# Performance work log

Hardware: AMD Instinct MI355X
Metric: run time of the kernel (lower is better)

Reference implementation:

```python
import jax, jax.numpy as jnp
import numpy as np

B, L, IN_DIM, DIM, H = 1, 256, 128, 32, 4
LN_EPS = 1e-5


def setup_inputs() -> dict:
    key = jax.random.key(0)
    ks = jax.random.split(key, 7)
    z = jax.random.normal(ks[0], (B, L, L, IN_DIM), dtype=jnp.float32)
    src_mask = jax.random.randint(ks[1], (B, L), 0, 2, dtype=jnp.int32)
    ln_g = jnp.ones((IN_DIM,), jnp.float32)
    ln_b = jnp.zeros((IN_DIM,), jnp.float32)
    w_qkv = jax.random.normal(ks[2], (IN_DIM, 3 * H * DIM), jnp.float32) * 0.02
    w_pair = jax.random.normal(ks[3], (IN_DIM, H), jnp.float32) * 0.02
    w_gate = jax.random.normal(ks[4], (IN_DIM, IN_DIM), jnp.float32) * 0.02
    b_gate = jnp.zeros((IN_DIM,), jnp.float32)
    w_out = jax.random.normal(ks[5], (H * DIM, IN_DIM), jnp.float32) * 0.02
    b_out = jnp.zeros((IN_DIM,), jnp.float32)
    return dict(z=z, src_mask=src_mask, ln_g=ln_g, ln_b=ln_b, w_qkv=w_qkv,
                w_pair=w_pair, w_gate=w_gate, b_gate=b_gate, w_out=w_out, b_out=b_out)


def reference(z, src_mask, ln_g, ln_b, w_qkv, w_pair, w_gate, b_gate, w_out, b_out):
    # mask: 0 -> -1, then outer product -> (B, L, L) with entries in {-1, +1}
    m = jnp.where(src_mask == 0, -1, src_mask).astype(jnp.float32)
    attn_mask = m[:, :, None] * m[:, None, :]                      # (B, L, L)

    # LayerNorm over feature dim (biased variance, as torch)
    mu = jnp.mean(z, axis=-1, keepdims=True)
    var = jnp.mean((z - mu) ** 2, axis=-1, keepdims=True)
    zn = (z - mu) / jnp.sqrt(var + LN_EPS) * ln_g + ln_b           # (B, I, J, C)

    gate = jax.nn.sigmoid(zn @ w_gate + b_gate)                    # (B, I, J, C)
    bias = zn @ w_pair                                             # (B, I, J, H)

    qkv = zn @ w_qkv                                               # (B, I, J, 3*H*D)
    q, k, v = jnp.split(qkv, 3, axis=-1)
    q = q.reshape(B, L, L, H, DIM)
    k = k.reshape(B, L, L, H, DIM)
    v = v.reshape(B, L, L, H, DIM)

    # NOTE: original code DIVIDES by scale = d**-0.5 (i.e. multiplies by sqrt(d)).
    scale = DIM ** (-0.5)
    logits = jnp.einsum('brihd,brjhd->brijh', q, k) / scale        # (B, R, I, J, H)
    logits = logits + bias[:, None, :, :, :]
    # NOTE: original masked_fill uses -1e-9 (tiny), kept faithfully.
    logits = jnp.where(attn_mask[:, None, :, :, None] == -1, jnp.float32(-1e-9), logits)
    attn = jax.nn.softmax(logits, axis=3)                          # softmax over key j

    out = jnp.einsum('brijh,brjhd->brihd', attn, v)                # (B, R, I, H, D)
    out = out.reshape(B, L, L, H * DIM)
    return (gate * out) @ w_out + b_out                            # (B, I, J, C)
```

## Files before the change

### kernel.cpp

```cpp
#include <hip/hip_runtime.h>
#include <hip/hip_bf16.h>

#define L_DIM 256
#define C_DIM 128
#define H_DIM 4
#define NPOS (L_DIM * L_DIM)
#define SQRT_D 5.6568542494923806f

typedef float f32x4 __attribute__((ext_vector_type(4)));
typedef short bf16x8 __attribute__((ext_vector_type(8)));
typedef unsigned short ushort8_t __attribute__((ext_vector_type(8)));

__device__ __forceinline__ float bf2f(unsigned short u) {
  return __uint_as_float(((unsigned)u) << 16);
}
__device__ __forceinline__ unsigned short f2bf(float f) {
  unsigned u = __float_as_uint(f);
  unsigned r = u + 0x7fffu + ((u >> 16) & 1u);
  return (unsigned short)(r >> 16);
}

__global__ __launch_bounds__(256)
void k_prep(const float* __restrict__ w_qkv, const float* __restrict__ w_gate,
            const float* __restrict__ w_out,
            unsigned short* __restrict__ WcS, unsigned short* __restrict__ WoT) {
  int idx = blockIdx.x * 256 + threadIdx.x;
  if (idx < 4 * 128 * 128) {
    int h = idx >> 14, rem = idx & 16383, rr = rem >> 7, c = rem & 127;
    int o = rr >> 5, n32 = rr & 31;
    float v = (o < 3) ? w_qkv[c * 384 + o * 128 + h * 32 + n32]
                      : w_gate[c * 128 + h * 32 + n32];
    int byte_in_row = (2 * c) ^ ((rr & 7) << 4);
    WcS[h * 16384 + rr * 128 + (byte_in_row >> 1)] = f2bf(v);
  } else if (idx < 4 * 128 * 128 + 128 * 128) {
    int i2 = idx - 65536;
    int n = i2 >> 7, c = i2 & 127;
    WoT[i2] = f2bf(w_out[c * 128 + n]);
  }
}

__global__ __launch_bounds__(256)
void k_bias(const float* __restrict__ z, const float* __restrict__ ln_g,
            const float* __restrict__ ln_b, const float* __restrict__ w_pair,
            float* __restrict__ biasT) {
  int t = threadIdx.x;
  int p = blockIdx.x * 32 + (t >> 3);
  int lane = t & 7;
  const float* zp = &z[(size_t)p * C_DIM + lane * 16];
  float x[16];
  #pragma unroll
  for (int e = 0; e < 4; e++) {
    float4 v = reinterpret_cast<const float4*>(zp)[e];
    x[e * 4 + 0] = v.x; x[e * 4 + 1] = v.y; x[e * 4 + 2] = v.z; x[e * 4 + 3] = v.w;
  }
  float s = 0.f;
  #pragma unroll
  for (int e = 0; e < 16; e++) s += x[e];
  s += __shfl_xor(s, 1); s += __shfl_xor(s, 2); s += __shfl_xor(s, 4);
  float mu = s * (1.0f / C_DIM);
  float v2 = 0.f;
  #pragma unroll
  for (int e = 0; e < 16; e++) { float d = x[e] - mu; v2 += d * d; }
  v2 += __shfl_xor(v2, 1); v2 += __shfl_xor(v2, 2); v2 += __shfl_xor(v2, 4);
  float rs = rsqrtf(v2 * (1.0f / C_DIM) + 1e-5f);
  float bh[H_DIM] = {};
  #pragma unroll
  for (int e = 0; e < 16; e++) {
    int c = lane * 16 + e;
    float zn = (x[e] - mu) * rs * ln_g[c] + ln_b[c];
    #pragma unroll
    for (int h = 0; h < H_DIM; h++) bh[h] += zn * w_pair[c * H_DIM + h];
  }
  #pragma unroll
  for (int h = 0; h < H_DIM; h++) {
    bh[h] += __shfl_xor(bh[h], 1); bh[h] += __shfl_xor(bh[h], 2); bh[h] += __shfl_xor(bh[h], 4);
  }
  if (lane == 0) {
    int iz = p >> 8, jz = p & 255;
    #pragma unroll
    for (int h = 0; h < H_DIM; h++) biasT[h * NPOS + jz * L_DIM + iz] = bh[h];
  }
}

__global__ __launch_bounds__(1024)
void k_fused(const float* __restrict__ z, const int* __restrict__ src_mask,
             const float* __restrict__ ln_g, const float* __restrict__ ln_b,
             const float* __restrict__ b_gate, const unsigned short* __restrict__ WcS,
             const float* __restrict__ biasT, float* __restrict__ og) {
  __shared__ __align__(16) char smem[156672];
  char* zn_c = smem;
  unsigned short* Qs = (unsigned short*)(smem);
  unsigned short* Ks = (unsigned short*)(smem + 20480);
  char* Vt_c = smem + 40960;
  char* P_c0 = smem + 57344;
  char* Wt_c = smem + 90112;
  int*  smk  = (int*)(smem + 155648);

  const int t = threadIdx.x;
  const int wave = t >> 6, lane = t & 63;
  const int l15 = lane & 15, l4 = lane >> 4;
  const int rbase = blockIdx.x * L_DIM;
  const int wrow0 = wave * 16;
  char* P_c = P_c0 + wave * 2048;

  {
    int ln8 = t & 7;
    #pragma unroll
    for (int pass = 0; pass < 2; ++pass) {
      int pos = pass * 128 + (t >> 3);
      const float* zp = z + ((size_t)(rbase + pos)) * C_DIM + ln8 * 16;
      float x[16];
      #pragma unroll
      for (int e = 0; e < 4; e++) {
        float4 v = reinterpret_cast<const float4*>(zp)[e];
        x[e * 4 + 0] = v.x; x[e * 4 + 1] = v.y; x[e * 4 + 2] = v.z; x[e * 4 + 3] = v.w;
      }
      float s = 0.f;
      #pragma unroll
      for (int e = 0; e < 16; e++) s += x[e];
      s += __shfl_xor(s, 1); s += __shfl_xor(s, 2); s += __shfl_xor(s, 4);
      float mu = s * (1.0f / C_DIM);
      float v2 = 0.f;
      #pragma unroll
      for (int e = 0; e < 16; e++) { float d = x[e] - mu; v2 += d * d; }
      v2 += __shfl_xor(v2, 1); v2 += __shfl_xor(v2, 2); v2 += __shfl_xor(v2, 4);
      float rstd = rsqrtf(v2 * (1.0f / C_DIM) + 1e-5f);
      unsigned short hb[16];
      #pragma unroll
      for (int e = 0; e < 16; e++) {
        int c = ln8 * 16 + e;
        hb[e] = f2bf((x[e] - mu) * rstd * ln_g[c] + ln_b[c]);
      }
      uint4 w0, w1;
      w0.x = hb[0] | ((unsigned)hb[1] << 16);  w0.y = hb[2] | ((unsigned)hb[3] << 16);
      w0.z = hb[4] | ((unsigned)hb[5] << 16);  w0.w = hb[6] | ((unsigned)hb[7] << 16);
      w1.x = hb[8] | ((unsigned)hb[9] << 16);  w1.y = hb[10] | ((unsigned)hb[11] << 16);
      w1.z = hb[12] | ((unsigned)hb[13] << 16); w1.w = hb[14] | ((unsigned)hb[15] << 16);
      int sw = (pos & 7) << 4;
      *(uint4*)(zn_c + pos * 256 + ((ln8 * 32) ^ sw)) = w0;
      *(uint4*)(zn_c + pos * 256 + ((ln8 * 32 + 16) ^ sw)) = w1;
    }
    if (t < 256) smk[t] = src_mask[t];
    const ushort8_t* src = (const ushort8_t*)WcS;
    ushort8_t* dst = (ushort8_t*)Wt_c;
    dst[t] = src[t];
    dst[t + 1024] = src[t + 1024];
  }
  __syncthreads();

  bf16x8 afr[4];
  {
    int row = wrow0 + l15, sw = (row & 7) << 4;
    #pragma unroll
    for (int kk = 0; kk < 4; kk++)
      afr[kk] = *(const bf16x8*)(zn_c + row * 256 + ((kk * 64 + l4 * 16) ^ sw));
  }
  unsigned mib = 0, mjb = 0;
  #pragma unroll
  for (int q = 0; q < 4; q++)
    if (smk[wrow0 + l4 * 4 + q] == 0) mib |= 1u << q;
  #pragma unroll
  for (int jj = 0; jj < 16; jj++)
    if (smk[(jj >> 2) * 64 + (jj & 3) * 16 + l15] == 0) mjb |= 1u << jj;
  __syncthreads();

  for (int h = 0; h < H_DIM; ++h) {
    const char* WtCur = Wt_c + (h & 1) * 32768;
    ushort8_t ld0, ld1;
    if (h < 3) {
      const ushort8_t* src = (const ushort8_t*)(WcS + (h + 1) * 16384);
      ld0 = src[t]; ld1 = src[t + 1024];
    }

    f32x4 gacc[2];
    #pragma unroll
    for (int o = 0; o < 4; o++) {
      #pragma unroll
      for (int nt = 0; nt < 2; nt++) {
        f32x4 acc = {0.f, 0.f, 0.f, 0.f};
        #pragma unroll
        for (int kk = 0; kk < 4; kk++) {
          int wr = o * 32 + nt * 16 + l15;
          bf16x8 bfr = *(const bf16x8*)(WtCur + wr * 256 + ((kk * 64 + l4 * 16) ^ ((wr & 7) << 4)));
          acc = __builtin_amdgcn_mfma_f32_16x16x32_bf16(afr[kk], bfr, acc, 0, 0, 0);
        }
        int colb = nt * 16 + l15;
        int rowb = wrow0 + l4 * 4;
        if (o == 0) {
          #pragma unroll
          for (int q = 0; q < 4; q++) Qs[(rowb + q) * 40 + colb] = f2bf(acc[q]);
        } else if (o == 1) {
          #pragma unroll
          for (int q = 0; q < 4; q++) Ks[(rowb + q) * 40 + colb] = f2bf(acc[q]);
        } else if (o == 2) {
          uint2 pv;
          pv.x = f2bf(acc[0]) | ((unsigned)f2bf(acc[1]) << 16);
          pv.y = f2bf(acc[2]) | ((unsigned)f2bf(acc[3]) << 16);
          *(uint2*)(Vt_c + colb * 512 + ((rowb * 2) ^ ((colb & 7) << 4))) = pv;
        } else {
          gacc[nt] = acc;
        }
      }
    }
    __syncthreads();

    bf16x8 qfr = *(const bf16x8*)((const char*)Qs + (wrow0 + l15) * 80 + l4 * 16);
    const float* biasTh = biasT + h * NPOS;
    float s_part[4] = {0.f, 0.f, 0.f, 0.f};
    f32x4 o_acc[2];
    o_acc[0] = (f32x4){0.f, 0.f, 0.f, 0.f};
    o_acc[1] = (f32x4){0.f, 0.f, 0.f, 0.f};

    for (int jb = 0; jb < 4; ++jb) {
      f32x4 sacc[4];
      #pragma unroll
      for (int ji = 0; ji < 4; ji++) {
        int jr = jb * 64 + ji * 16 + l15;
        bf16x8 kfr = *(const bf16x8*)((const char*)Ks + jr * 80 + l4 * 16);
        f32x4 zz = {0.f, 0.f, 0.f, 0.f};
        sacc[ji] = __builtin_amdgcn_mfma_f32_16x16x32_bf16(qfr, kfr, zz, 0, 0, 0);
      }
      #pragma unroll
      for (int ji = 0; ji < 4; ji++) {
        int j = jb * 64 + ji * 16 + l15;
        int ib = wrow0 + l4 * 4;
        float4 b4 = *(const float4*)(biasTh + j * L_DIM + ib);
        bool mjz = (mjb >> (jb * 4 + ji)) & 1u;
        float bb[4] = {b4.x, b4.y, b4.z, b4.w};
        #pragma unroll
        for (int q = 0; q < 4; q++) {
          float sv = sacc[ji][q] * SQRT_D + bb[q];
          bool miz = (mib >> q) & 1u;
          if (miz != mjz) sv = -1e-9f;
          float p = __expf(sv);
          s_part[q] += p;
          int il = l4 * 4 + q, jl = ji * 16 + l15;
          *(unsigned short*)(P_c + il * 128 + ((jl * 2) ^ ((il & 7) << 4))) = f2bf(p);
        }
      }
      #pragma unroll
      for (int kk = 0; kk < 2; kk++) {
        bf16x8 pfr = *(const bf16x8*)(P_c + l15 * 128 + ((kk * 64 + l4 * 16) ^ ((l15 & 7) << 4)));
        #pragma unroll
        for (int nd = 0; nd < 2; nd++) {
          int vr = nd * 16 + l15;
          bf16x8 vfr = *(const bf16x8*)(Vt_c + vr * 512 +
                                        ((jb * 128 + kk * 64 + l4 * 16) ^ ((vr & 7) << 4)));
          o_acc[nd] = __builtin_amdgcn_mfma_f32_16x16x32_bf16(pfr, vfr, o_acc[nd], 0, 0, 0);
        }
      }
    }

    #pragma unroll
    for (int q = 0; q < 4; q++) {
      float s = s_part[q];
      s += __shfl_xor(s, 1); s += __shfl_xor(s, 2);
      s += __shfl_xor(s, 4); s += __shfl_xor(s, 8);
      s_part[q] = s;
    }

    #pragma unroll
    for (int nd = 0; nd < 2; nd++) {
      int c = h * 32 + nd * 16 + l15;
      float bg = b_gate[c];
      #pragma unroll
      for (int q = 0; q < 4; q++) {
        float g = 1.0f / (1.0f + __expf(-(gacc[nd][q] + bg)));
        float ov = o_acc[nd][q] * (1.0f / s_part[q]) * g;
        int p = rbase + wrow0 + l4 * 4 + q;
        og[(size_t)p * C_DIM + c] = ov;
      }
    }

    if (h < 3) {
      ushort8_t* dst = (ushort8_t*)(Wt_c + ((h + 1) & 1) * 32768);
      dst[t] = ld0;
      dst[t + 1024] = ld1;
    }
    __syncthreads();
  }
}

__global__ __launch_bounds__(256)
void k_out(const unsigned short* __restrict__ WoT, const float* __restrict__ b_out,
           float* __restrict__ out) {
  __shared__ __align__(16) char smem[49152];
  char* Ab_c  = smem;
  char* WoT_c = smem + 16384;
  int t = threadIdx.x;
  int gr0 = blockIdx.x * 64;
  #pragma unroll
  for (int e = 0; e < 8; e++) {
    int f = t + e * 256;
    int row = f >> 5, c4 = f & 31;
    float4 v = *(const float4*)(out + (size_t)(gr0 + row) * C_DIM + c4 * 4);
    uint2 pv;
    pv.x = f2bf(v.x) | ((unsigned)f2bf(v.y) << 16);
    pv.y = f2bf(v.z) | ((unsigned)f2bf(v.w) << 16);
    *(uint2*)(Ab_c + row * 256 + ((c4 * 8) ^ ((row & 7) << 4))) = pv;
  }
  {
    int row = t >> 1, seg = t & 1;
    const char* gsrc = (const char*)(WoT + row * 128);
    int sw = (row & 7) << 4;
    #pragma unroll
    for (int e = 0; e < 8; e++) {
      int cb = seg * 128 + e * 16;
      ushort8_t v = *(const ushort8_t*)(gsrc + cb);
      *(ushort8_t*)(WoT_c + row * 256 + (cb ^ sw)) = v;
    }
  }
  __syncthreads();

  int wave = t >> 6, lane = t & 63;
  int base = wave * 16;
  bf16x8 afr[4];
  #pragma unroll
  for (int kk = 0; kk < 4; kk++) {
    int row = base + (lane & 15);
    int cb = kk * 64 + (lane >> 4) * 16;
    afr[kk] = *(const bf16x8*)(Ab_c + row * 256 + (cb ^ ((row & 7) << 4)));
  }
  f32x4 acc[8];
  #pragma unroll
  for (int nt = 0; nt < 8; nt++) {
    acc[nt] = (f32x4){0.f, 0.f, 0.f, 0.f};
    #pragma unroll
    for (int kk = 0; kk < 4; kk++) {
      int wr = nt * 16 + (lane & 15);
      int cb = kk * 64 + (lane >> 4) * 16;
      bf16x8 bfr = *(const bf16x8*)(WoT_c + wr * 256 + (cb ^ ((wr & 7) << 4)));
      acc[nt] = __builtin_amdgcn_mfma_f32_16x16x32_bf16(afr[kk], bfr, acc[nt], 0, 0, 0);
    }
  }
  __syncthreads();
  #pragma unroll
  for (int nt = 0; nt < 8; nt++) {
    int n = nt * 16 + (lane & 15);
    float bo = b_out[n];
    #pragma unroll
    for (int q = 0; q < 4; q++) {
      int p = gr0 + base + (lane >> 4) * 4 + q;
      out[(size_t)p * C_DIM + n] = acc[nt][q] + bo;
    }
  }
}

extern "C" void kernel_launch(void* const* d_in, const int* in_sizes, int n_in,
                              void* d_out, int out_size, void* d_ws, size_t ws_size,
                              hipStream_t stream) {
  const float* z      = (const float*)d_in[0];
  const int*   smask  = (const int*)  d_in[1];
  const float* ln_g   = (const float*)d_in[2];
  const float* ln_b   = (const float*)d_in[3];
  const float* w_qkv  = (const float*)d_in[4];
  const float* w_pair = (const float*)d_in[5];
  const float* w_gate = (const float*)d_in[6];
  const float* b_gate = (const float*)d_in[7];
  const float* w_out  = (const float*)d_in[8];
  const float* b_out  = (const float*)d_in[9];
  float* out = (float*)d_out;

  char* ws = (char*)d_ws;
  unsigned short* WcS   = (unsigned short*)(ws);
  unsigned short* WoT   = (unsigned short*)(ws + 131072);
  float*          biasT = (float*)(ws + 163840);
  (void)ws_size; (void)in_sizes; (void)n_in; (void)out_size;

  k_prep<<<dim3(320), dim3(256), 0, stream>>>(w_qkv, w_gate, w_out, WcS, WoT);
  k_bias<<<dim3(NPOS / 32), dim3(256), 0, stream>>>(z, ln_g, ln_b, w_pair, biasT);
  k_fused<<<dim3(L_DIM), dim3(1024), 0, stream>>>(z, smask, ln_g, ln_b, b_gate, WcS, biasT, out);
  k_out<<<dim3(NPOS / 64), dim3(256), 0, stream>>>(WoT, b_out, out);
}
```

Before: 192.1 us.

## Fuse output projection into attention kernel and drop separate k_out pass

Removes the k_out kernel. The gated attention output is now kept in registers as packed bf16, staged per wave into shared memory, and multiplied by a pre-swizzled W_out that is prefetched into the weight double buffer during the last head iteration. This avoids writing and re-reading the full fp32 intermediate through global memory and saves one kernel launch. The bias layout also changes from transposed to natural order with a simpler coalesced write, so the fused kernel now does scalar bias loads instead of float4 loads. The launch bounds gain a min-blocks hint, which may raise register pressure alongside the 16 extra live registers.

Result: slower. 211.4 us (+10.1%).

```diff
diff --git a/kernel.cpp b/kernel.cpp
--- a/kernel.cpp
+++ b/kernel.cpp
@@ -23,7 +23,7 @@
 __global__ __launch_bounds__(256)
 void k_prep(const float* __restrict__ w_qkv, const float* __restrict__ w_gate,
             const float* __restrict__ w_out,
-            unsigned short* __restrict__ WcS, unsigned short* __restrict__ WoT) {
+            unsigned short* __restrict__ WcS, unsigned short* __restrict__ WoS) {
   int idx = blockIdx.x * 256 + threadIdx.x;
   if (idx < 4 * 128 * 128) {
     int h = idx >> 14, rem = idx & 16383, rr = rem >> 7, c = rem & 127;
@@ -35,14 +35,15 @@
   } else if (idx < 4 * 128 * 128 + 128 * 128) {
     int i2 = idx - 65536;
     int n = i2 >> 7, c = i2 & 127;
-    WoT[i2] = f2bf(w_out[c * 128 + n]);
+    int byte_in_row = (2 * c) ^ ((n & 7) << 4);
+    WoS[n * 128 + (byte_in_row >> 1)] = f2bf(w_out[c * 128 + n]);
   }
 }
 
 __global__ __launch_bounds__(256)
 void k_bias(const float* __restrict__ z, const float* __restrict__ ln_g,
             const float* __restrict__ ln_b, const float* __restrict__ w_pair,
-            float* __restrict__ biasT) {
+            float* __restrict__ biasN) {
   int t = threadIdx.x;
   int p = blockIdx.x * 32 + (t >> 3);
   int lane = t & 7;
@@ -75,18 +76,15 @@
   for (int h = 0; h < H_DIM; h++) {
     bh[h] += __shfl_xor(bh[h], 1); bh[h] += __shfl_xor(bh[h], 2); bh[h] += __shfl_xor(bh[h], 4);
   }
-  if (lane == 0) {
-    int iz = p >> 8, jz = p & 255;
-    #pragma unroll
-    for (int h = 0; h < H_DIM; h++) biasT[h * NPOS + jz * L_DIM + iz] = bh[h];
-  }
-}
-
-__global__ __launch_bounds__(1024)
+  if (lane < H_DIM) biasN[lane * NPOS + p] = bh[lane];
+}
+
+__global__ __launch_bounds__(1024, 4)
 void k_fused(const float* __restrict__ z, const int* __restrict__ src_mask,
              const float* __restrict__ ln_g, const float* __restrict__ ln_b,
              const float* __restrict__ b_gate, const unsigned short* __restrict__ WcS,
-             const float* __restrict__ biasT, float* __restrict__ og) {
+             const unsigned short* __restrict__ WoS, const float* __restrict__ biasN,
+             const float* __restrict__ b_out, float* __restrict__ out) {
   __shared__ __align__(16) char smem[156672];
   char* zn_c = smem;
   unsigned short* Qs = (unsigned short*)(smem);
@@ -164,11 +162,14 @@
     if (smk[(jj >> 2) * 64 + (jj & 3) * 16 + l15] == 0) mjb |= 1u << jj;
   __syncthreads();
 
+  unsigned og_pk[16];
+
   for (int h = 0; h < H_DIM; ++h) {
     const char* WtCur = Wt_c + (h & 1) * 32768;
     ushort8_t ld0, ld1;
-    if (h < 3) {
-      const ushort8_t* src = (const ushort8_t*)(WcS + (h + 1) * 16384);
+    {
+      const ushort8_t* src = (h < 3) ? (const ushort8_t*)(WcS + (h + 1) * 16384)
+                                     : (const ushort8_t*)WoS;
       ld0 = src[t]; ld1 = src[t + 1024];
     }
 
@@ -205,7 +206,7 @@
     __syncthreads();
 
     bf16x8 qfr = *(const bf16x8*)((const char*)Qs + (wrow0 + l15) * 80 + l4 * 16);
-    const float* biasTh = biasT + h * NPOS;
+    const float* biasNh = biasN + h * NPOS;
     float s_part[4] = {0.f, 0.f, 0.f, 0.f};
     f32x4 o_acc[2];
     o_acc[0] = (f32x4){0.f, 0.f, 0.f, 0.f};
@@ -222,14 +223,12 @@
       }
       #pragma unroll
       for (int ji = 0; ji < 4; ji++) {
-        int j = jb * 64 + ji * 16 + l15;
-        int ib = wrow0 + l4 * 4;
-        float4 b4 = *(const float4*)(biasTh + j * L_DIM + ib);
+        int jcol = jb * 64 + ji * 16 + l15;
         bool mjz = (mjb >> (jb * 4 + ji)) & 1u;
-        float bb[4] = {b4.x, b4.y, b4.z, b4.w};
         #pragma unroll
         for (int q = 0; q < 4; q++) {
-          float sv = sacc[ji][q] * SQRT_D + bb[q];
+          float bb = biasNh[(wrow0 + l4 * 4 + q) * L_DIM + jcol];
+          float sv = sacc[ji][q] * SQRT_D + bb;
           bool miz = (mib >> q) & 1u;
           if (miz != mjz) sv = -1e-9f;
           float p = __expf(sv);
@@ -263,85 +262,62 @@
     for (int nd = 0; nd < 2; nd++) {
       int c = h * 32 + nd * 16 + l15;
       float bg = b_gate[c];
+      unsigned short pk[4];
       #pragma unroll
       for (int q = 0; q < 4; q++) {
         float g = 1.0f / (1.0f + __expf(-(gacc[nd][q] + bg)));
-        float ov = o_acc[nd][q] * (1.0f / s_part[q]) * g;
-        int p = rbase + wrow0 + l4 * 4 + q;
-        og[(size_t)p * C_DIM + c] = ov;
-      }
-    }
-
-    if (h < 3) {
+        pk[q] = f2bf(o_acc[nd][q] * (1.0f / s_part[q]) * g);
+      }
+      og_pk[(h * 2 + nd) * 2 + 0] = pk[0] | ((unsigned)pk[1] << 16);
+      og_pk[(h * 2 + nd) * 2 + 1] = pk[2] | ((unsigned)pk[3] << 16);
+    }
+
+    {
       ushort8_t* dst = (ushort8_t*)(Wt_c + ((h + 1) & 1) * 32768);
       dst[t] = ld0;
       dst[t + 1024] = ld1;
     }
     __syncthreads();
   }
-}
-
-__global__ __launch_bounds__(256)
-void k_out(const unsigned short* __restrict__ WoT, const float* __restrict__ b_out,
-           float* __restrict__ out) {
-  __shared__ __align__(16) char smem[49152];
-  char* Ab_c  = smem;
-  char* WoT_c = smem + 16384;
-  int t = threadIdx.x;
-  int gr0 = blockIdx.x * 64;
-  #pragma unroll
-  for (int e = 0; e < 8; e++) {
-    int f = t + e * 256;
-    int row = f >> 5, c4 = f & 31;
-    float4 v = *(const float4*)(out + (size_t)(gr0 + row) * C_DIM + c4 * 4);
-    uint2 pv;
-    pv.x = f2bf(v.x) | ((unsigned)f2bf(v.y) << 16);
-    pv.y = f2bf(v.z) | ((unsigned)f2bf(v.w) << 16);
-    *(uint2*)(Ab_c + row * 256 + ((c4 * 8) ^ ((row & 7) << 4))) = pv;
-  }
+
   {
-    int row = t >> 1, seg = t & 1;
-    const char* gsrc = (const char*)(WoT + row * 128);
-    int sw = (row & 7) << 4;
-    #pragma unroll
-    for (int e = 0; e < 8; e++) {
-      int cb = seg * 128 + e * 16;
-      ushort8_t v = *(const ushort8_t*)(gsrc + cb);
-      *(ushort8_t*)(WoT_c + row * 256 + (cb ^ sw)) = v;
-    }
-  }
-  __syncthreads();
-
-  int wave = t >> 6, lane = t & 63;
-  int base = wave * 16;
-  bf16x8 afr[4];
-  #pragma unroll
-  for (int kk = 0; kk < 4; kk++) {
-    int row = base + (lane & 15);
-    int cb = kk * 64 + (lane >> 4) * 16;
-    afr[kk] = *(const bf16x8*)(Ab_c + row * 256 + (cb ^ ((row & 7) << 4)));
-  }
-  f32x4 acc[8];
-  #pragma unroll
-  for (int nt = 0; nt < 8; nt++) {
-    acc[nt] = (f32x4){0.f, 0.f, 0.f, 0.f};
-    #pragma unroll
-    for (int kk = 0; kk < 4; kk++) {
-      int wr = nt * 16 + (lane & 15);
-      int cb = kk * 64 + (lane >> 4) * 16;
-      bf16x8 bfr = *(const bf16x8*)(WoT_c + wr * 256 + (cb ^ ((wr & 7) << 4)));
-      acc[nt] = __builtin_amdgcn_mfma_f32_16x16x32_bf16(afr[kk], bfr, acc[nt], 0, 0, 0);
-    }
-  }
-  __syncthreads();
-  #pragma unroll
-  for (int nt = 0; nt < 8; nt++) {
-    int n = nt * 16 + (lane & 15);
-    float bo = b_out[n];
-    #pragma unroll
-    for (int q = 0; q < 4; q++) {
-      int p = gr0 + base + (lane >> 4) * 4 + q;
-      out[(size_t)p * C_DIM + n] = acc[nt][q] + bo;
+    char* ogt = smem + wave * 4096;
+    #pragma unroll
+    for (int h2 = 0; h2 < 4; h2++) {
+      #pragma unroll
+      for (int nd = 0; nd < 2; nd++) {
+        int c2 = h2 * 32 + nd * 16 + l15;
+        unsigned ua = og_pk[(h2 * 2 + nd) * 2 + 0];
+        unsigned ub = og_pk[(h2 * 2 + nd) * 2 + 1];
+        int r0 = l4 * 4;
+        *(unsigned short*)(ogt + (r0 + 0) * 256 + ((2 * c2) ^ (((r0 + 0) & 7) << 4))) = (unsigned short)(ua & 0xffff);
+        *(unsigned short*)(ogt + (r0 + 1) * 256 + ((2 * c2) ^ (((r0 + 1) & 7) << 4))) = (unsigned short)(ua >> 16);
+        *(unsigned short*)(ogt + (r0 + 2) * 256 + ((2 * c2) ^ (((r0 + 2) & 7) << 4))) = (unsigned short)(ub & 0xffff);
+        *(unsigned short*)(ogt + (r0 + 3) * 256 + ((2 * c2) ^ (((r0 + 3) & 7) << 4))) = (unsigned short)(ub >> 16);
+      }
+    }
+    bf16x8 afr2[4];
+    {
+      int row = l15, sw = (row & 7) << 4;
+      #pragma unroll
+      for (int kk = 0; kk < 4; kk++)
+        afr2[kk] = *(const bf16x8*)(ogt + row * 256 + ((kk * 64 + l4 * 16) ^ sw));
+    }
+    const char* WoS_c = Wt_c;
+    #pragma unroll
+    for (int nt = 0; nt < 8; nt++) {
+      f32x4 a2 = {0.f, 0.f, 0.f, 0.f};
+      #pragma unroll
+      for (int kk = 0; kk < 4; kk++) {
+        int wr = nt * 16 + l15;
+        bf16x8 bfr = *(const bf16x8*)(WoS_c + wr * 256 + ((kk * 64 + l4 * 16) ^ ((wr & 7) << 4)));
+        a2 = __builtin_amdgcn_mfma_f32_16x16x32_bf16(afr2[kk], bfr, a2, 0, 0, 0);
+      }
+      int n = nt * 16 + l15;
+      float bo = b_out[n];
+      #pragma unroll
+      for (int q = 0; q < 4; q++)
+        out[(size_t)(rbase + wrow0 + l4 * 4 + q) * C_DIM + n] = a2[q] + bo;
     }
   }
 }
@@ -363,12 +339,12 @@
 
   char* ws = (char*)d_ws;
   unsigned short* WcS   = (unsigned short*)(ws);
-  unsigned short* WoT   = (unsigned short*)(ws + 131072);
-  float*          biasT = (float*)(ws + 163840);
+  unsigned short* WoS   = (unsigned short*)(ws + 131072);
+  float*          biasN = (float*)(ws + 163840);
   (void)ws_size; (void)in_sizes; (void)n_in; (void)out_size;
 
-  k_prep<<<dim3(320), dim3(256), 0, stream>>>(w_qkv, w_gate, w_out, WcS, WoT);
-  k_bias<<<dim3(NPOS / 32), dim3(256), 0, stream>>>(z, ln_g, ln_b, w_pair, biasT);
-  k_fused<<<dim3(L_DIM), dim3(1024), 0, stream>>>(z, smask, ln_g, ln_b, b_gate, WcS, biasT, out);
-  k_out<<<dim3(NPOS / 64), dim3(256), 0, stream>>>(WoT, b_out, out);
-}
+  k_prep<<<dim3(320), dim3(256), 0, stream>>>(w_qkv, w_gate, w_out, WcS, WoS);
+  k_bias<<<dim3(NPOS / 32), dim3(256), 0, stream>>>(z, ln_g, ln_b, w_pair, biasN);
+  k_fused<<<dim3(L_DIM), dim3(1024), 0, stream>>>(z, smask, ln_g, ln_b, b_gate, WcS, WoS,
+                                                  biasN, b_out, out);
+}
```
